# Optimization experiments

Measured on AMD Instinct MI355X. Metric: run time of the kernel, lower is better.

Reference implementation:

```python
import jax, jax.numpy as jnp
import numpy as np

# ---- module constants (from init_kwargs) ----
W, H = 320, 240
VOXEL_SIZE = 0.05
DEPTH_MIN = 0.1 / VOXEL_SIZE          # 2.0  (voxel units, as in the torch module)
DEPTH_MAX = 4.0 / VOXEL_SIZE          # 80.0
STEP = 0.5                            # ray_increment = voxel_size/2 -> half a voxel in grid units
N_STEPS = int((DEPTH_MAX - DEPTH_MIN) / STEP)   # 156 ray-march steps
IGNORE = -1                           # config.data.ignore_label
DX, DY, DZ = 192, 192, 96             # dims3d (x, y, z); occ3d stored [B, Dz, Dy, Dx]
N_VOX, C_FEAT = 80000, 128
B, V = 1, 2


def setup_inputs() -> dict:
    key = jax.random.key(0)
    k1, k2, k3, k4 = jax.random.split(key, 4)
    features_3d = jax.random.normal(k1, (N_VOX, C_FEAT), dtype=jnp.float32)
    # occupied-voxel coordinates scattered into dense index grid (SparseTensor.dense())
    xi = jax.random.randint(k2, (N_VOX,), 0, DX)
    yi = jax.random.randint(k3, (N_VOX,), 0, DY)
    zi = jax.random.randint(k4, (N_VOX,), 0, DZ)
    occ3d = jnp.full((B, DZ, DY, DX), IGNORE, dtype=jnp.int32)
    occ3d = occ3d.at[0, zi, yi, xi].set(jnp.arange(N_VOX, dtype=jnp.int32))
    # camera-to-grid poses: identity rotation, camera inside grid looking +z
    vm = jnp.tile(jnp.eye(4, dtype=jnp.float32)[None, None], (B, V, 1, 1))
    trans = jnp.array([[96.0, 96.0, 2.0], [80.0, 100.0, 3.0]], dtype=jnp.float32)
    vm = vm.at[:, :, :3, 3].set(trans[None])
    intr = jnp.tile(jnp.array([280.0, 280.0, 160.0, 120.0], dtype=jnp.float32)[None, None], (B, V, 1))
    return {"features_3d": features_3d, "view_matrix": vm,
            "intrinsic_params": intr, "occ3d": occ3d}


_CORNERS = [(dz, dy, dx) for dz in (0, 1) for dy in (0, 1) for dx in (0, 1)]


def _corner_lookup(occ3d, base, bb):
    """Gather the 8 corner voxel indices around base [..., 3] = (x, y, z)."""
    Dz, Dy, Dx = occ3d.shape[1:]
    idxs, valids = [], []
    for dz, dy, dx in _CORNERS:
        cx = base[..., 0] + dx
        cy = base[..., 1] + dy
        cz = base[..., 2] + dz
        inb = (cx >= 0) & (cx < Dx) & (cy >= 0) & (cy < Dy) & (cz >= 0) & (cz < Dz)
        idx = occ3d[bb, jnp.clip(cz, 0, Dz - 1), jnp.clip(cy, 0, Dy - 1), jnp.clip(cx, 0, Dx - 1)]
        idxs.append(idx)
        valids.append(inb & (idx != IGNORE))
    return idxs, valids


def reference(features_3d, view_matrix, intrinsic_params, occ3d):
    Bv, Vv = view_matrix.shape[:2]
    N, C = features_3d.shape
    fx = intrinsic_params[..., 0][..., None, None]   # [B,V,1,1]
    fy = intrinsic_params[..., 1][..., None, None]
    cx = intrinsic_params[..., 2][..., None, None]
    cy = intrinsic_params[..., 3][..., None, None]
    u = jnp.arange(W, dtype=jnp.float32) + 0.5
    v = jnp.arange(H, dtype=jnp.float32) + 0.5
    uu, vv = jnp.meshgrid(u, v)                      # [H,W]
    dirs_cam = jnp.stack([(uu[None, None] - cx) / fx,
                          (vv[None, None] - cy) / fy,
                          jnp.broadcast_to(jnp.float32(1.0), (Bv, Vv, H, W))], axis=-1)  # [B,V,H,W,3]
    R = view_matrix[..., :3, :3]
    t = view_matrix[..., :3, 3]
    dirs = jnp.einsum('bvij,bvhwj->bvhwi', R, dirs_cam)   # ray dirs in grid space
    origin = t[:, :, None, None, :]
    bb = jnp.arange(Bv)[:, None, None, None]               # batch index, broadcasts

    hit0 = jnp.zeros((Bv, Vv, H, W), dtype=bool)
    base0 = jnp.zeros((Bv, Vv, H, W, 3), dtype=jnp.int32)
    frac0 = jnp.zeros((Bv, Vv, H, W, 3), dtype=jnp.float32)
    depths = DEPTH_MIN + STEP * jnp.arange(N_STEPS, dtype=jnp.float32)

    def step(carry, d):
        hit, base, frac = carry
        p = origin + d * dirs - 0.5                        # corner-interp frame
        b0 = jnp.floor(p).astype(jnp.int32)
        fr = (p - b0).astype(jnp.float32)
        _, valids = _corner_lookup(occ3d, b0, bb)
        occ_any = valids[0]
        for vd in valids[1:]:
            occ_any = occ_any | vd
        new = occ_any & (~hit)                             # first-hit semantics
        base = jnp.where(new[..., None], b0, base)
        frac = jnp.where(new[..., None], fr, frac)
        return (hit | occ_any, base, frac), None

    (hit, base, frac), _ = jax.lax.scan(step, (hit0, base0, frac0), depths)

    idxs, valids = _corner_lookup(occ3d, base, bb)
    hitf = hit.astype(jnp.float32)
    fxw, fyw, fzw = frac[..., 0], frac[..., 1], frac[..., 2]
    ws = []
    for k, (dz, dy, dx) in enumerate(_CORNERS):
        w = ((fzw if dz else 1.0 - fzw) *
             (fyw if dy else 1.0 - fyw) *
             (fxw if dx else 1.0 - fxw))
        ws.append(w * valids[k].astype(jnp.float32) * hitf)
    wsum = ws[0]
    for w in ws[1:]:
        wsum = wsum + w
    inv = 1.0 / (wsum + 1e-8)

    projected = jnp.zeros((Bv, Vv, H, W, C), dtype=jnp.float32)
    norm_ws, masked_idx = [], []
    for k in range(8):
        w = ws[k] * inv
        norm_ws.append(w)
        projected = projected + w[..., None] * features_3d[jnp.clip(idxs[k], 0, N - 1)]
        masked_idx.append(jnp.where(valids[k] & hit, idxs[k], IGNORE))

    indexes_image = jnp.stack(masked_idx, axis=-1)         # [B,V,H,W,8]
    vox_dist_weights = jnp.stack(norm_ws, axis=-1)         # [B,V,H,W,8]

    flat_idx = indexes_image.reshape(-1)
    contrib = (flat_idx != IGNORE).astype(jnp.float32)
    mapping3dto2d_num = jax.ops.segment_sum(contrib, jnp.clip(flat_idx, 0, N - 1), num_segments=N)

    return projected, indexes_image, vox_dist_weights, mapping3dto2d_num
```

## Files before the change

kernel.cpp:

```cpp
#include <hip/hip_runtime.h>
#include <limits.h>

#define W_IMG 320
#define H_IMG 240
#define N_VIEW 2
#define DX_ 192
#define DY_ 192
#define DZ_ 96
#define NVOX 80000
#define CFEAT 128
#define NSTEPS 156
#define NPIX (N_VIEW * H_IMG * W_IMG)

#define NCELLS (DZ_ * DY_ * DX_)
#define WPR (DX_ / 32)
#define NWORDS (NCELLS / 32)

#define OFF_PROJ 0
#define OFF_IDX  (NPIX * CFEAT)
#define OFF_W    (OFF_IDX + NPIX * 8)
#define OFF_MAP  (OFF_W + NPIX * 8)

#define WS_COPIES_OFF 442368

#define GATHER_BLOCKS (NPIX * 32 / 256)

__global__ __launch_bounds__(256) void dilate_direct_kernel(
    const int* __restrict__ occ, unsigned* __restrict__ dil,
    float* __restrict__ zero_tgt, int zero_n4)
{
    int w = blockIdx.x * 256 + threadIdx.x;
    int zt = w * 2;
    if (zt < zero_n4)     ((float4*)zero_tgt)[zt]     = make_float4(0.f, 0.f, 0.f, 0.f);
    if (zt + 1 < zero_n4) ((float4*)zero_tgt)[zt + 1] = make_float4(0.f, 0.f, 0.f, 0.f);
    if (w >= NWORDS) return;

    int wx = w % WPR;
    int y  = (w / WPR) % DY_;
    int z  = w / (WPR * DY_);
    unsigned acc = 0;
    #pragma unroll
    for (int dz = 0; dz < 2; ++dz) {
        int zz = z + dz;
        if (zz >= DZ_) continue;
        #pragma unroll
        for (int dy = 0; dy < 2; ++dy) {
            int yy = y + dy;
            if (yy >= DY_) continue;
            const int* row = occ + (zz * DY_ + yy) * DX_ + (wx << 5);
            const int4* r4 = (const int4*)row;
            unsigned m = 0;
            #pragma unroll
            for (int k = 0; k < 8; ++k) {
                int4 q = r4[k];
                unsigned b = (unsigned)(q.x != -1)
                           | ((unsigned)(q.y != -1) << 1)
                           | ((unsigned)(q.z != -1) << 2)
                           | ((unsigned)(q.w != -1) << 3);
                m |= b << (k * 4);
            }
            unsigned nxt = (wx + 1 < WPR) ? (unsigned)(row[32] != -1) : 0u;
            acc |= m | (m >> 1) | (nxt << 31);
        }
    }
    dil[w] = acc;
}

__device__ __forceinline__ bool slow_any(const int* __restrict__ occ,
                                         int ix, int iy, int iz)
{
    bool any = false;
    #pragma unroll
    for (int c = 0; c < 8; ++c) {
        int ddz = c >> 2, ddy = (c >> 1) & 1, ddx = c & 1;
        int cxl = ix + ddx, cyl = iy + ddy, czl = iz + ddz;
        bool inb = ((unsigned)cxl < DX_) & ((unsigned)cyl < DY_) & ((unsigned)czl < DZ_);
        int xc = min(max(cxl, 0), DX_ - 1);
        int yc = min(max(cyl, 0), DY_ - 1);
        int zc = min(max(czl, 0), DZ_ - 1);
        int idx = occ[(zc * DY_ + yc) * DX_ + xc];
        any = any | (inb & (idx != -1));
    }
    return any;
}

__global__ __launch_bounds__(256) void raycast_kernel(
    const float* __restrict__ vm,
    const float* __restrict__ intr,
    const int*   __restrict__ occ,
    const unsigned* __restrict__ dil,
    float* __restrict__ out_idx,
    float* __restrict__ out_w,
    float* __restrict__ map_base,
    int copy_mask)
{
    int t    = blockIdx.x * 256 + threadIdx.x;
    int pix  = t >> 2;
    int sub  = t & 3;
    int lane = threadIdx.x & 63;

    int v   = pix / (H_IMG * W_IMG);
    int rem = pix - v * (H_IMG * W_IMG);
    int h   = rem / W_IMG;
    int w   = rem - h * W_IMG;

    const float* M = vm + v * 16;
    const float* I = intr + v * 4;
    float fx = I[0], fy = I[1], cx = I[2], cy = I[3];
    float uu = (float)w + 0.5f;
    float vv = (float)h + 0.5f;
    float dc0 = __fdiv_rn(__fsub_rn(uu, cx), fx);
    float dc1 = __fdiv_rn(__fsub_rn(vv, cy), fy);
    float dc2 = 1.0f;
    float dir0 = __fadd_rn(__fadd_rn(__fmul_rn(M[0], dc0), __fmul_rn(M[1], dc1)), __fmul_rn(M[2], dc2));
    float dir1 = __fadd_rn(__fadd_rn(__fmul_rn(M[4], dc0), __fmul_rn(M[5], dc1)), __fmul_rn(M[6], dc2));
    float dir2 = __fadd_rn(__fadd_rn(__fmul_rn(M[8], dc0), __fmul_rn(M[9], dc1)), __fmul_rn(M[10], dc2));
    float t0 = M[3], t1 = M[7], t2 = M[11];

    int s_hit = INT_MAX;
    for (int base = 0; base < NSTEPS; base += 32) {
        int smin = INT_MAX;
        int need = 0;
        #pragma unroll
        for (int j = 0; j < 8; ++j) {
            int s = base + sub + 4 * j;
            float d  = __fadd_rn(2.0f, __fmul_rn(0.5f, (float)s));
            float px = __fsub_rn(__fadd_rn(t0, __fmul_rn(d, dir0)), 0.5f);
            float py = __fsub_rn(__fadd_rn(t1, __fmul_rn(d, dir1)), 0.5f);
            float pz = __fsub_rn(__fadd_rn(t2, __fmul_rn(d, dir2)), 0.5f);
            int ix = (int)floorf(px);
            int iy = (int)floorf(py);
            int iz = (int)floorf(pz);
            bool inb3 = ((unsigned)ix < DX_) & ((unsigned)iy < DY_) & ((unsigned)iz < DZ_);
            int addr = inb3 ? ((iz * DY_ + iy) * WPR + (ix >> 5)) : 0;
            unsigned wd = dil[addr];
            bool ok = (s < NSTEPS);
            bool any = ok & inb3 & (bool)((wd >> (ix & 31)) & 1u);
            bool ns  = ok & !inb3 & (ix >= -1) & (ix < DX_) & (iy >= -1) & (iy < DY_)
                          & (iz >= -1) & (iz < DZ_);
            need |= (ns ? 1 : 0) << j;
            if (any) smin = min(smin, s);
        }
        if (__builtin_expect(need, 0)) {
            for (int j = 0; j < 8; ++j) {
                if ((need >> j) & 1) {
                    int s = base + sub + 4 * j;
                    float d  = __fadd_rn(2.0f, __fmul_rn(0.5f, (float)s));
                    float px = __fsub_rn(__fadd_rn(t0, __fmul_rn(d, dir0)), 0.5f);
                    float py = __fsub_rn(__fadd_rn(t1, __fmul_rn(d, dir1)), 0.5f);
                    float pz = __fsub_rn(__fadd_rn(t2, __fmul_rn(d, dir2)), 0.5f);
                    int ix = (int)floorf(px);
                    int iy = (int)floorf(py);
                    int iz = (int)floorf(pz);
                    if (slow_any(occ, ix, iy, iz)) smin = min(smin, s);
                }
            }
        }
        smin = min(smin, __shfl_xor(smin, 1));
        smin = min(smin, __shfl_xor(smin, 2));
        if (smin != INT_MAX) { s_hit = smin; break; }
    }

    int hit = 0;
    int bx = 0, by = 0, bz = 0;
    float fr0 = 0.f, fr1 = 0.f, fr2 = 0.f;
    if (s_hit != INT_MAX) {
        hit = 1;
        float d  = __fadd_rn(2.0f, __fmul_rn(0.5f, (float)s_hit));
        float px = __fsub_rn(__fadd_rn(t0, __fmul_rn(d, dir0)), 0.5f);
        float py = __fsub_rn(__fadd_rn(t1, __fmul_rn(d, dir1)), 0.5f);
        float pz = __fsub_rn(__fadd_rn(t2, __fmul_rn(d, dir2)), 0.5f);
        float fpx = floorf(px), fpy = floorf(py), fpz = floorf(pz);
        bx = (int)fpx; by = (int)fpy; bz = (int)fpz;
        fr0 = px - fpx; fr1 = py - fpy; fr2 = pz - fpz;
    }

    float ws8[8];
    int   id8[8];
    float wsum = 0.0f;
    #pragma unroll
    for (int c = 0; c < 8; ++c) {
        float wk = 0.0f;
        int idv = -1;
        if (hit) {
            int ddz = c >> 2, ddy = (c >> 1) & 1, ddx = c & 1;
            int cxl = bx + ddx, cyl = by + ddy, czl = bz + ddz;
            bool inb = ((unsigned)cxl < DX_) & ((unsigned)cyl < DY_) & ((unsigned)czl < DZ_);
            int xc = min(max(cxl, 0), DX_ - 1);
            int yc = min(max(cyl, 0), DY_ - 1);
            int zc = min(max(czl, 0), DZ_ - 1);
            int idx = occ[(zc * DY_ + yc) * DX_ + xc];
            bool valid = inb & (idx != -1);
            float gw = ddz ? fr2 : (1.0f - fr2);
            gw = __fmul_rn(gw, ddy ? fr1 : (1.0f - fr1));
            gw = __fmul_rn(gw, ddx ? fr0 : (1.0f - fr0));
            if (valid) { wk = gw; idv = idx; }
        }
        ws8[c] = wk;
        id8[c] = idv;
        wsum = __fadd_rn(wsum, wk);
    }
    float inv = __fdiv_rn(1.0f, __fadd_rn(wsum, 1e-8f));

    float wn[8];
    #pragma unroll
    for (int c = 0; c < 8; ++c) wn[c] = __fmul_rn(ws8[c], inv);

    float4* w4 = (float4*)out_w;
    float4* i4 = (float4*)out_idx;
    if (sub == 0)      w4[pix * 2]     = make_float4(wn[0], wn[1], wn[2], wn[3]);
    else if (sub == 1) w4[pix * 2 + 1] = make_float4(wn[4], wn[5], wn[6], wn[7]);
    else if (sub == 2) i4[pix * 2]     = make_float4((float)id8[0], (float)id8[1], (float)id8[2], (float)id8[3]);
    else               i4[pix * 2 + 1] = make_float4((float)id8[4], (float)id8[5], (float)id8[6], (float)id8[7]);

    float* mymap = map_base + (int)(blockIdx.x & copy_mask) * NVOX;
    #pragma unroll
    for (int c = 0; c < 8; ++c) {
        int vid  = id8[c];
        int prev = __shfl(vid, max(lane - 4, 0));
        bool leader = (lane < 4) || (vid != prev);
        unsigned long long lm = __ballot(leader);
        int gl = lane & ~3;
        unsigned long long higher = (gl == 60) ? 0ULL : (lm >> (gl + 4));
        int cnt = higher ? (((__ffsll(higher) - 1) >> 2) + 1) : ((64 - gl) >> 2);
        if (sub == 0 && leader && vid >= 0) atomicAdd(&mymap[vid], (float)cnt);
    }
}

__global__ __launch_bounds__(256) void gather_reduce_kernel(
    const float* __restrict__ feat,
    const float* __restrict__ out_idx,
    const float* __restrict__ out_w,
    float* __restrict__ proj,
    const float* __restrict__ copies,
    float* __restrict__ out_map,
    int nc)
{
    if (blockIdx.x >= GATHER_BLOCKS) {
        if (nc > 0) {
            int t = (blockIdx.x - GATHER_BLOCKS) * 256 + threadIdx.x;
            if (t < NVOX / 4) {
                const float4* c4 = (const float4*)copies;
                float4 s = c4[t];
                for (int c = 1; c < nc; ++c) {
                    float4 a = c4[c * (NVOX / 4) + t];
                    s.x += a.x; s.y += a.y; s.z += a.z; s.w += a.w;
                }
                ((float4*)out_map)[t] = s;
            }
        }
        return;
    }
    int t = blockIdx.x * 256 + threadIdx.x;
    int pix  = t >> 5;
    int lane = t & 31;

    const float4* f4 = (const float4*)feat;
    float4 acc = make_float4(0.f, 0.f, 0.f, 0.f);
    #pragma unroll
    for (int c = 0; c < 8; ++c) {
        float wk = out_w[pix * 8 + c];
        if (wk != 0.0f) {
            int idx = (int)out_idx[pix * 8 + c];
            float4 f = f4[idx * (CFEAT / 4) + lane];
            acc.x += wk * f.x;
            acc.y += wk * f.y;
            acc.z += wk * f.z;
            acc.w += wk * f.w;
        }
    }
    ((float4*)proj)[pix * (CFEAT / 4) + lane] = acc;
}

extern "C" void kernel_launch(void* const* d_in, const int* in_sizes, int n_in,
                              void* d_out, int out_size, void* d_ws, size_t ws_size,
                              hipStream_t stream) {
    const float* feat = (const float*)d_in[0];
    const float* vm   = (const float*)d_in[1];
    const float* intr = (const float*)d_in[2];
    const int*   occ  = (const int*)d_in[3];
    float* out = (float*)d_out;

    float* out_proj = out + OFF_PROJ;
    float* out_idx  = out + OFF_IDX;
    float* out_w    = out + OFF_W;
    float* out_map  = out + OFF_MAP;

    unsigned* dil = (unsigned*)d_ws;
    float* copies = (float*)((char*)d_ws + WS_COPIES_OFF);

    size_t avail = ws_size > WS_COPIES_OFF ? ws_size - WS_COPIES_OFF : 0;
    int nc = (int)(avail / (NVOX * sizeof(float)));
    nc = nc >= 8 ? 8 : (nc >= 4 ? 4 : (nc >= 2 ? 2 : (nc >= 1 ? 1 : 0)));

    float* map_base = nc ? copies : out_map;
    int copy_mask   = nc ? nc - 1 : 0;
    float* zero_tgt = nc ? copies : out_map;
    int zero_n4     = (nc ? nc : 1) * (NVOX / 4);

    dilate_direct_kernel<<<(NWORDS + 255) / 256, 256, 0, stream>>>(
        occ, dil, zero_tgt, zero_n4);

    raycast_kernel<<<(NPIX * 4) / 256, 256, 0, stream>>>(
        vm, intr, occ, dil, out_idx, out_w, map_base, copy_mask);

    int reduce_blocks = (NVOX / 4 + 255) / 256;
    gather_reduce_kernel<<<GATHER_BLOCKS + reduce_blocks, 256, 0, stream>>>(
        feat, out_idx, out_w, out_proj, copies, out_map, nc);
}
```

Before: 59.62 us.

## Split dilation rows across lanes and drop replicated histogram copies

```diff
diff --git a/kernel.cpp b/kernel.cpp
--- a/kernel.cpp
+++ b/kernel.cpp
@@ -21,49 +21,43 @@
 #define OFF_W    (OFF_IDX + NPIX * 8)
 #define OFF_MAP  (OFF_W + NPIX * 8)
 
-#define WS_COPIES_OFF 442368
-
 #define GATHER_BLOCKS (NPIX * 32 / 256)
 
-__global__ __launch_bounds__(256) void dilate_direct_kernel(
+__global__ __launch_bounds__(256) void dilate_v2_kernel(
     const int* __restrict__ occ, unsigned* __restrict__ dil,
-    float* __restrict__ zero_tgt, int zero_n4)
-{
-    int w = blockIdx.x * 256 + threadIdx.x;
-    int zt = w * 2;
-    if (zt < zero_n4)     ((float4*)zero_tgt)[zt]     = make_float4(0.f, 0.f, 0.f, 0.f);
-    if (zt + 1 < zero_n4) ((float4*)zero_tgt)[zt + 1] = make_float4(0.f, 0.f, 0.f, 0.f);
-    if (w >= NWORDS) return;
-
+    float* __restrict__ out_map)
+{
+    int g = blockIdx.x * 256 + threadIdx.x;
+    if (g < NVOX / 4) ((float4*)out_map)[g] = make_float4(0.f, 0.f, 0.f, 0.f);
+
+    int w = g >> 2;
+    int q = g & 3;
     int wx = w % WPR;
     int y  = (w / WPR) % DY_;
     int z  = w / (WPR * DY_);
+    int zz = z + (q >> 1);
+    int yy = y + (q & 1);
+
     unsigned acc = 0;
-    #pragma unroll
-    for (int dz = 0; dz < 2; ++dz) {
-        int zz = z + dz;
-        if (zz >= DZ_) continue;
+    if (zz < DZ_ && yy < DY_) {
+        const int* row = occ + (zz * DY_ + yy) * DX_ + (wx << 5);
+        const int4* r4 = (const int4*)row;
+        unsigned m = 0;
         #pragma unroll
-        for (int dy = 0; dy < 2; ++dy) {
-            int yy = y + dy;
-            if (yy >= DY_) continue;
-            const int* row = occ + (zz * DY_ + yy) * DX_ + (wx << 5);
-            const int4* r4 = (const int4*)row;
-            unsigned m = 0;
-            #pragma unroll
-            for (int k = 0; k < 8; ++k) {
-                int4 q = r4[k];
-                unsigned b = (unsigned)(q.x != -1)
-                           | ((unsigned)(q.y != -1) << 1)
-                           | ((unsigned)(q.z != -1) << 2)
-                           | ((unsigned)(q.w != -1) << 3);
-                m |= b << (k * 4);
-            }
-            unsigned nxt = (wx + 1 < WPR) ? (unsigned)(row[32] != -1) : 0u;
-            acc |= m | (m >> 1) | (nxt << 31);
-        }
-    }
-    dil[w] = acc;
+        for (int k = 0; k < 8; ++k) {
+            int4 qd = r4[k];
+            unsigned b = (unsigned)(qd.x != -1)
+                       | ((unsigned)(qd.y != -1) << 1)
+                       | ((unsigned)(qd.z != -1) << 2)
+                       | ((unsigned)(qd.w != -1) << 3);
+            m |= b << (k * 4);
+        }
+        unsigned nxt = (wx + 1 < WPR) ? (unsigned)(row[32] != -1) : 0u;
+        acc = m | (m >> 1) | (nxt << 31);
+    }
+    acc |= __shfl_xor(acc, 1);
+    acc |= __shfl_xor(acc, 2);
+    if (q == 0) dil[w] = acc;
 }
 
 __device__ __forceinline__ bool slow_any(const int* __restrict__ occ,
@@ -91,8 +85,7 @@
     const unsigned* __restrict__ dil,
     float* __restrict__ out_idx,
     float* __restrict__ out_w,
-    float* __restrict__ map_base,
-    int copy_mask)
+    float* __restrict__ out_map)
 {
     int t    = blockIdx.x * 256 + threadIdx.x;
     int pix  = t >> 2;
@@ -213,7 +206,6 @@
     else if (sub == 2) i4[pix * 2]     = make_float4((float)id8[0], (float)id8[1], (float)id8[2], (float)id8[3]);
     else               i4[pix * 2 + 1] = make_float4((float)id8[4], (float)id8[5], (float)id8[6], (float)id8[7]);
 
-    float* mymap = map_base + (int)(blockIdx.x & copy_mask) * NVOX;
     #pragma unroll
     for (int c = 0; c < 8; ++c) {
         int vid  = id8[c];
@@ -223,34 +215,16 @@
         int gl = lane & ~3;
         unsigned long long higher = (gl == 60) ? 0ULL : (lm >> (gl + 4));
         int cnt = higher ? (((__ffsll(higher) - 1) >> 2) + 1) : ((64 - gl) >> 2);
-        if (sub == 0 && leader && vid >= 0) atomicAdd(&mymap[vid], (float)cnt);
-    }
-}
-
-__global__ __launch_bounds__(256) void gather_reduce_kernel(
+        if (sub == 0 && leader && vid >= 0) atomicAdd(&out_map[vid], (float)cnt);
+    }
+}
+
+__global__ __launch_bounds__(256) void gather_kernel(
     const float* __restrict__ feat,
     const float* __restrict__ out_idx,
     const float* __restrict__ out_w,
-    float* __restrict__ proj,
-    const float* __restrict__ copies,
-    float* __restrict__ out_map,
-    int nc)
-{
-    if (blockIdx.x >= GATHER_BLOCKS) {
-        if (nc > 0) {
-            int t = (blockIdx.x - GATHER_BLOCKS) * 256 + threadIdx.x;
-            if (t < NVOX / 4) {
-                const float4* c4 = (const float4*)copies;
-                float4 s = c4[t];
-                for (int c = 1; c < nc; ++c) {
-                    float4 a = c4[c * (NVOX / 4) + t];
-                    s.x += a.x; s.y += a.y; s.z += a.z; s.w += a.w;
-                }
-                ((float4*)out_map)[t] = s;
-            }
-        }
-        return;
-    }
+    float* __restrict__ proj)
+{
     int t = blockIdx.x * 256 + threadIdx.x;
     int pix  = t >> 5;
     int lane = t & 31;
@@ -287,24 +261,12 @@
     float* out_map  = out + OFF_MAP;
 
     unsigned* dil = (unsigned*)d_ws;
-    float* copies = (float*)((char*)d_ws + WS_COPIES_OFF);
-
-    size_t avail = ws_size > WS_COPIES_OFF ? ws_size - WS_COPIES_OFF : 0;
-    int nc = (int)(avail / (NVOX * sizeof(float)));
-    nc = nc >= 8 ? 8 : (nc >= 4 ? 4 : (nc >= 2 ? 2 : (nc >= 1 ? 1 : 0)));
-
-    float* map_base = nc ? copies : out_map;
-    int copy_mask   = nc ? nc - 1 : 0;
-    float* zero_tgt = nc ? copies : out_map;
-    int zero_n4     = (nc ? nc : 1) * (NVOX / 4);
-
-    dilate_direct_kernel<<<(NWORDS + 255) / 256, 256, 0, stream>>>(
-        occ, dil, zero_tgt, zero_n4);
+
+    dilate_v2_kernel<<<(NWORDS * 4) / 256, 256, 0, stream>>>(occ, dil, out_map);
 
     raycast_kernel<<<(NPIX * 4) / 256, 256, 0, stream>>>(
-        vm, intr, occ, dil, out_idx, out_w, map_base, copy_mask);
-
-    int reduce_blocks = (NVOX / 4 + 255) / 256;
-    gather_reduce_kernel<<<GATHER_BLOCKS + reduce_blocks, 256, 0, stream>>>(
-        feat, out_idx, out_w, out_proj, copies, out_map, nc);
-}
+        vm, intr, occ, dil, out_idx, out_w, out_map);
+
+    gather_kernel<<<GATHER_BLOCKS, 256, 0, stream>>>(
+        feat, out_idx, out_w, out_proj);
+}
```

Result: slower. 87.33 us (+46.5%).
